# Kernel tuning notes

Measured on AMD Instinct MI355X. Metric: run time of the kernel, lower is better.

The kernel has to match this reference:

```python
import jax, jax.numpy as jnp
import numpy as np

B, S, D = 2, 4096, 1024
H, DK, DV = 4, 128, 256          # head_k_dim, head_v_dim
KD, VD = H * DK, H * DV          # key_dim=512, value_dim=1024
RANK = 16                        # gate_low_rank_dim
GLN = 16.0                       # gate_logit_normalizer
EPS = 1e-5
C = 64                           # chunk size
NC = S // C


def setup_inputs() -> dict:
    key = jax.random.key(0)
    ks = jax.random.split(key, 9)
    w = lambda k, shape: (jax.random.normal(k, shape, jnp.float32) * 0.02)
    return {
        "x": jax.random.normal(ks[0], (B, S, D), jnp.float32),
        "Wq": w(ks[1], (D, KD)),
        "Wk": w(ks[2], (D, KD)),
        "Wv": w(ks[3], (D, VD)),
        "Wgk1": w(ks[4], (D, RANK)),
        "Wgk2": w(ks[5], (RANK, KD)),
        "bgk": jnp.zeros((KD,), jnp.float32),
        "Wg": w(ks[6], (D, VD)),
        "Wo": w(ks[7], (VD, D)),
        "norm_w": jnp.ones((DV,), jnp.float32),
    }


def _gla_chunk(q, k, v, gk):
    """Chunkwise gated linear attention. q,k,gk: [B,S,H,DK]; v: [B,S,H,DV]."""
    qc = q.reshape(B, NC, C, H, DK)
    kc = k.reshape(B, NC, C, H, DK)
    vc = v.reshape(B, NC, C, H, DV)
    gc = gk.reshape(B, NC, C, H, DK)
    gcum = jnp.cumsum(gc, axis=2)                       # inclusive within-chunk cumsum (<= 0)
    g_last = gcum[:, :, -1]                             # [B,NC,H,DK]
    q_t = qc * jnp.exp(gcum)                            # q decayed forward
    k_inv = kc * jnp.exp(-gcum)                         # for intra-chunk scores
    k_dec = kc * jnp.exp(g_last[:, :, None] - gcum)     # for state update (bounded)
    # intra-chunk causal scores
    A = jnp.einsum('bnthk,bnshk->bnhts', q_t, k_inv)    # [B,NC,H,C,C]
    mask = jnp.tril(jnp.ones((C, C), bool))
    A = jnp.where(mask, A, 0.0)
    o_intra = jnp.einsum('bnhts,bnshv->bnthv', A, vc)   # [B,NC,C,H,DV]
    # per-chunk state contribution
    kv = jnp.einsum('bnthk,bnthv->bnhkv', k_dec, vc)    # [B,NC,H,DK,DV]

    def step(state, inp):
        q_tc, gl, kvc = inp                             # [B,C,H,DK], [B,H,DK], [B,H,DK,DV]
        o_inter = jnp.einsum('bthk,bhkv->bthv', q_tc, state)
        state = state * jnp.exp(gl)[..., None] + kvc
        return state, o_inter

    xs = (jnp.swapaxes(q_t, 0, 1), jnp.swapaxes(g_last, 0, 1), jnp.swapaxes(kv, 0, 1))
    init = jnp.zeros((B, H, DK, DV), q.dtype)
    _, o_inter = jax.lax.scan(step, init, xs)           # [NC,B,C,H,DV]
    o = o_intra + jnp.swapaxes(o_inter, 0, 1)
    return o.reshape(B, S, H, DV)


def reference(x, Wq, Wk, Wv, Wgk1, Wgk2, bgk, Wg, Wo, norm_w):
    scale = DK ** -0.5
    q = (x @ Wq).reshape(B, S, H, DK) * scale
    k = (x @ Wk).reshape(B, S, H, DK)
    v = (x @ Wv).reshape(B, S, H, DV)
    gk = (jax.nn.log_sigmoid((x @ Wgk1) @ Wgk2 + bgk) / GLN).reshape(B, S, H, DK)
    o = _gla_chunk(q, k, v, gk)                          # [B,S,H,DV]
    # fused RMSNorm + swish gate (per-head norm over DV)
    g = (x @ Wg).reshape(B, S, H, DV)
    o = o * jax.lax.rsqrt(jnp.mean(o * o, axis=-1, keepdims=True) + EPS) * norm_w
    o = o * (g * jax.nn.sigmoid(g))
    return o.reshape(B, S, VD) @ Wo
```

## Files before the change

kernel.cpp:

```cpp
#include <hip/hip_runtime.h>

typedef __bf16 bf16_t;
typedef __bf16 bf16x4 __attribute__((ext_vector_type(4)));
typedef __bf16 bf16x8 __attribute__((ext_vector_type(8)));
typedef float  f32x4  __attribute__((ext_vector_type(4)));

#define MFMA16(a,b,c) __builtin_amdgcn_mfma_f32_16x16x32_bf16((a),(b),(c),0,0,0)

#define SCALE_Q 0.08838834764831845f

#define GLOBAL_LOAD_LDS16(gptr, lptr)                                          \
  __builtin_amdgcn_global_load_lds(                                            \
      (const __attribute__((address_space(1))) void*)(gptr),                   \
      (__attribute__((address_space(3))) void*)(lptr), 16, 0, 0)

struct ConvSrcs {
  const void *wq, *wk, *wv, *wg, *wo, *gk1, *gk2, *bgk, *nw;
};
__device__ __forceinline__ void convT_tile(const void* src, bf16_t* dst,
                                           int Ccols, int bx, int by,
                                           bool isf32, bf16_t (*t)[33]) {
  int tx = threadIdx.x & 31, ty = threadIdx.x >> 5;
  int r0 = by * 32, c0 = bx * 32;
#pragma unroll
  for (int i = 0; i < 4; i++) {
    int r = r0 + ty + i * 8, cc = c0 + tx;
    float v = isf32 ? ((const float*)src)[(size_t)r * Ccols + cc]
                    : (float)((const bf16_t*)src)[(size_t)r * Ccols + cc];
    t[ty + i * 8][tx] = (bf16_t)v;
  }
  __syncthreads();
#pragma unroll
  for (int i = 0; i < 4; i++) {
    int cc = c0 + ty + i * 8;
    dst[(size_t)cc * 1024 + r0 + tx] = t[tx][ty + i * 8];
  }
}
__device__ __forceinline__ void conv_straight(const void* src, bf16_t* dst,
                                              int base_blk, int n, bool isf32) {
  int g = (blockIdx.x - base_blk) * 256 + threadIdx.x;
  int i = g * 8;
  if (i >= n) return;
  if (isf32) {
    const float4* s = (const float4*)src;
    float4 a = s[g * 2], b = s[g * 2 + 1];
    bf16x8 o;
    o[0] = (bf16_t)a.x; o[1] = (bf16_t)a.y; o[2] = (bf16_t)a.z; o[3] = (bf16_t)a.w;
    o[4] = (bf16_t)b.x; o[5] = (bf16_t)b.y; o[6] = (bf16_t)b.z; o[7] = (bf16_t)b.w;
    *(bf16x8*)(dst + i) = o;
  } else {
    *(bf16x8*)(dst + i) = ((const bf16x8*)src)[g];
  }
}
__global__ __launch_bounds__(256) void k_convW(ConvSrcs s,
                                               const unsigned int* __restrict__ nwp,
                                               bf16_t* __restrict__ tWcat,
                                               bf16_t* __restrict__ tWo,
                                               bf16_t* __restrict__ cWgk1,
                                               bf16_t* __restrict__ cWgk2,
                                               bf16_t* __restrict__ cbgk,
                                               bf16_t* __restrict__ cnw) {
  __shared__ bf16_t t[32][33];
  bool isf32 = (nwp[0] == 0x3F800000u);
  int blk = blockIdx.x;
  if (blk < 512) {
    convT_tile(s.wq, tWcat, 512, blk & 15, blk >> 4, isf32, t);
  } else if (blk < 1024) {
    int b2 = blk - 512;
    convT_tile(s.wk, tWcat + (size_t)512 * 1024, 512, b2 & 15, b2 >> 4, isf32, t);
  } else if (blk < 2048) {
    int b2 = blk - 1024;
    convT_tile(s.wv, tWcat + (size_t)1024 * 1024, 1024, b2 & 31, b2 >> 5, isf32, t);
  } else if (blk < 3072) {
    int b2 = blk - 2048;
    convT_tile(s.wg, tWcat + (size_t)2048 * 1024, 1024, b2 & 31, b2 >> 5, isf32, t);
  } else if (blk < 4096) {
    int b2 = blk - 3072;
    convT_tile(s.wo, tWo, 1024, b2 & 31, b2 >> 5, isf32, t);
  } else if (blk < 4104) {
    conv_straight(s.gk1, cWgk1, 4096, 16384, isf32);
  } else if (blk < 4108) {
    conv_straight(s.gk2, cWgk2, 4104, 8192, isf32);
  } else if (blk == 4108) {
    conv_straight(s.bgk, cbgk, 4108, 512, isf32);
  } else {
    conv_straight(s.nw, cnw, 4109, 256, isf32);
  }
}

__global__ __launch_bounds__(256) void k_gk1c(const void* __restrict__ src,
                                              const unsigned int* __restrict__ nwp,
                                              const bf16_t* __restrict__ W1,
                                              float* __restrict__ tmp,
                                              bf16_t* __restrict__ cx) {
  bool isf32 = (nwp[0] == 0x3F800000u);
  int wave = threadIdx.x >> 6, lane = threadIdx.x & 63;
  int m = blockIdx.x * 4 + wave;
  float p[16];
#pragma unroll
  for (int n = 0; n < 16; n++) p[n] = 0.f;
  for (int kk = 0; kk < 16; kk++) {
    int k = kk * 64 + lane;
    float raw = isf32 ? ((const float*)src)[(size_t)m * 1024 + k]
                      : (float)((const bf16_t*)src)[(size_t)m * 1024 + k];
    bf16_t bx = (bf16_t)raw;
    cx[(size_t)m * 1024 + k] = bx;
    float xv = (float)bx;
    bf16x8 w0 = *(const bf16x8*)(W1 + k * 16);
    bf16x8 w1 = *(const bf16x8*)(W1 + k * 16 + 8);
#pragma unroll
    for (int j = 0; j < 8; j++) {
      p[j]     += xv * (float)w0[j];
      p[8 + j] += xv * (float)w1[j];
    }
  }
#pragma unroll
  for (int off = 1; off < 64; off <<= 1) {
#pragma unroll
    for (int n = 0; n < 16; n++) p[n] += __shfl_xor(p[n], off, 64);
  }
#pragma unroll
  for (int n = 0; n < 16; n++)
    if (lane == n) tmp[(size_t)m * 16 + n] = p[n];
}

__global__ __launch_bounds__(128) void k_gkcum(const float* __restrict__ tmp,
                                               const bf16_t* __restrict__ W2,
                                               const bf16_t* __restrict__ bgk,
                                               float* __restrict__ gcum,
                                               float* __restrict__ glast,
                                               float* __restrict__ eglast) {
  __shared__ float lt[64][16];
  int blk = blockIdx.x;
  int bh = blk >> 6, n = blk & 63;
  int b = bh >> 2, h = bh & 3;
  int dk = threadIdx.x;
  int m0 = b * 4096 + n * 64;
  const float4* tsrc = (const float4*)(tmp + (size_t)m0 * 16);
  ((float4*)lt)[dk * 2]     = tsrc[dk * 2];
  ((float4*)lt)[dk * 2 + 1] = tsrc[dk * 2 + 1];
  int col = h * 128 + dk;
  float wv[16];
#pragma unroll
  for (int k = 0; k < 16; k++) wv[k] = (float)W2[k * 512 + col];
  float bv = (float)bgk[col];
  __syncthreads();
  float run = 0.f;
  float* dst = gcum + ((size_t)bh * 4096 + (size_t)n * 64) * 128 + dk;
  for (int t = 0; t < 64; t++) {
    float acc = 0.f;
#pragma unroll
    for (int k = 0; k < 16; k++) acc += lt[t][k] * wv[k];
    float z = acc + bv;
    float lg = -__logf(1.f + __expf(-z)) * (1.f / 16.f);
    run += fmaxf(lg, -4.0f);
    dst[t * 128] = run;
  }
  glast[(size_t)blk * 128 + dk] = run;
  eglast[(size_t)blk * 128 + dk] = __expf(run);
}

__global__ __launch_bounds__(512, 4) void k_gemm(const bf16_t* __restrict__ Ag,
                                              const bf16_t* __restrict__ Bt,
                                              int mode,
                                              const float* __restrict__ gcum,
                                              const float* __restrict__ glast,
                                              bf16_t* __restrict__ qt,
                                              bf16_t* __restrict__ kinv,
                                              bf16_t* __restrict__ kdecT,
                                              bf16_t* __restrict__ vrT,
                                              bf16_t* __restrict__ gmat,
                                              float* __restrict__ fout) {
  __shared__ __attribute__((aligned(16))) bf16_t As[2 * 256 * 32];
  __shared__ __attribute__((aligned(16))) bf16_t Bs[2 * 128 * 32];
  int tid = threadIdx.x;
  int w = tid >> 6, lane = tid & 63, quad = lane >> 4, c = lane & 15;
  int bid = blockIdx.x;
  int xcd = bid & 7, slot = bid >> 3;
  int bm, bn;
  if (mode == 0) { bm = xcd * 4 + slot / 24; bn = slot % 24; }
  else           { bm = xcd * 4 + (slot >> 3); bn = slot & 7; }
  int m0 = bm * 256, n0 = bn * 128;
  int WM = w >> 1, WN = w & 1;
  int r0s = w * 32 + (lane >> 2);
  int r1s = r0s + 16;
  int rbs = w * 16 + (lane >> 2);
  int s = lane & 3;
  int f0 = (s - (r0s >> 1)) & 3;
  int f1 = (s - (r1s >> 1)) & 3;
  int fb = (s - (rbs >> 1)) & 3;
  const bf16_t* a0 = Ag + (size_t)(m0 + r0s) * 1024 + f0 * 8;
  const bf16_t* a1 = Ag + (size_t)(m0 + r1s) * 1024 + f1 * 8;
  const bf16_t* b0 = Bt + (size_t)(n0 + rbs) * 1024 + fb * 8;
  bf16_t* lA = As + w * 1024;
  bf16_t* lB = Bs + w * 512;
  int raOff[4], rbOff[4];
#pragma unroll
  for (int t4 = 0; t4 < 4; t4++) {
    int ra = WM * 64 + t4 * 16 + c;
    raOff[t4] = ra * 32 + (((quad + (ra >> 1)) & 3) * 8);
    int rb = WN * 64 + t4 * 16 + c;
    rbOff[t4] = rb * 32 + (((quad + (rb >> 1)) & 3) * 8);
  }
  GLOBAL_LOAD_LDS16(a0, lA);
  GLOBAL_LOAD_LDS16(a1, lA + 512);
  GLOBAL_LOAD_LDS16(b0, lB);
  f32x4 acc[4][4] = {};
  for (int k0 = 0; k0 < 1024; k0 += 32) {
    __syncthreads();
    int cur = (k0 >> 5) & 1;
    int nxt = cur ^ 1;
    if (k0 + 32 < 1024) {
      GLOBAL_LOAD_LDS16(a0 + k0 + 32, lA + nxt * 8192);
      GLOBAL_LOAD_LDS16(a1 + k0 + 32, lA + nxt * 8192 + 512);
      GLOBAL_LOAD_LDS16(b0 + k0 + 32, lB + nxt * 4096);
    }
    bf16x8 af[4], bfr[4];
#pragma unroll
    for (int t4 = 0; t4 < 4; t4++) af[t4] = *(const bf16x8*)(As + cur * 8192 + raOff[t4]);
#pragma unroll
    for (int t4 = 0; t4 < 4; t4++) bfr[t4] = *(const bf16x8*)(Bs + cur * 4096 + rbOff[t4]);
#pragma unroll
    for (int mt = 0; mt < 4; mt++)
#pragma unroll
      for (int nt = 0; nt < 4; nt++)
        acc[mt][nt] = MFMA16(af[mt], bfr[nt], acc[mt][nt]);
  }
#pragma unroll
  for (int mt = 0; mt < 4; mt++)
#pragma unroll
    for (int nt = 0; nt < 4; nt++) {
      int mb = m0 + WM * 64 + mt * 16 + quad * 4;
      int n  = n0 + WN * 64 + nt * 16 + c;
      if (mode == 1) {
#pragma unroll
        for (int r = 0; r < 4; r++)
          fout[(size_t)(mb + r) * 1024 + n] = acc[mt][nt][r];
      } else if (n0 < 512) {
        int b = mb >> 12, ss0 = mb & 4095, h = n >> 7, dk = n & 127;
        size_t idx0 = ((size_t)(b * 4 + h) * 4096 + ss0) * 128 + dk;
#pragma unroll
        for (int r = 0; r < 4; r++)
          qt[idx0 + (size_t)r * 128] =
              (bf16_t)(acc[mt][nt][r] * SCALE_Q * __expf(gcum[idx0 + (size_t)r * 128]));
      } else if (n0 < 1024) {
        int nk = n - 512;
        int b = mb >> 12, ss0 = mb & 4095, h = nk >> 7, dk = nk & 127;
        int bh = b * 4 + h, chunk = ss0 >> 6, t0 = ss0 & 63;
        size_t idx0 = ((size_t)bh * 4096 + ss0) * 128 + dk;
        float gl = glast[((size_t)bh * 64 + chunk) * 128 + dk];
        bf16x4 kd;
#pragma unroll
        for (int r = 0; r < 4; r++) {
          float gc = gcum[idx0 + (size_t)r * 128];
          kinv[idx0 + (size_t)r * 128] =
              (bf16_t)(acc[mt][nt][r] * __expf(fminf(-gc, 30.f)));
          kd[r] = (bf16_t)(acc[mt][nt][r] * __expf(gl - gc));
        }
        *(bf16x4*)(kdecT + ((size_t)(bh * 64 + chunk) * 128 + dk) * 64 + t0) = kd;
      } else if (n0 < 2048) {
        int nv = n - 1024;
        int b = mb >> 12, ss0 = mb & 4095, h = nv >> 8, dv = nv & 255;
        int bh = b * 4 + h, chunk = ss0 >> 6, t0 = ss0 & 63;
        bf16x4 vv;
#pragma unroll
        for (int r = 0; r < 4; r++) vv[r] = (bf16_t)acc[mt][nt][r];
        *(bf16x4*)(vrT + ((size_t)(bh * 64 + chunk) * 256 + dv) * 64 + t0) = vv;
      } else {
#pragma unroll
        for (int r = 0; r < 4; r++)
          gmat[(size_t)(mb + r) * 1024 + (n - 2048)] = (bf16_t)acc[mt][nt][r];
      }
    }
}

__global__ __launch_bounds__(512, 4) void k_kv(const bf16_t* __restrict__ kdecT,
                                               const bf16_t* __restrict__ vrT,
                                               bf16_t* __restrict__ kv) {
  int blk = blockIdx.x;
  int tid = threadIdx.x, wave = tid >> 6, lane = tid & 63;
  int quad = lane >> 4, c = lane & 15;
  size_t cb = (size_t)blk * 8192;
  size_t cv = (size_t)blk * 16384;
  size_t sb = (size_t)blk * 32768;
  int dvbase = (wave >> 1) * 64;
  int kgbase = (wave & 1) * 64;
  f32x4 acc[4][4] = {};
  for (int kk = 0; kk < 64; kk += 32) {
    bf16x8 a[4], bb[4];
#pragma unroll
    for (int mt = 0; mt < 4; mt++)
      a[mt] = *(const bf16x8*)(vrT + cv + (size_t)(dvbase + mt * 16 + c) * 64 + kk + quad * 8);
#pragma unroll
    for (int nt = 0; nt < 4; nt++)
      bb[nt] = *(const bf16x8*)(kdecT + cb + (size_t)(kgbase + nt * 16 + c) * 64 + kk + quad * 8);
#pragma unroll
    for (int mt = 0; mt < 4; mt++)
#pragma unroll
      for (int nt = 0; nt < 4; nt++)
        acc[mt][nt] = MFMA16(a[mt], bb[nt], acc[mt][nt]);
  }
#pragma unroll
  for (int mt = 0; mt < 4; mt++)
#pragma unroll
    for (int nt = 0; nt < 4; nt++)
#pragma unroll
      for (int r = 0; r < 4; r++) {
        int dv = dvbase + mt * 16 + quad * 4 + r;
        int kg = kgbase + nt * 16 + c;
        kv[sb + (size_t)dv * 128 + kg] = (bf16_t)acc[mt][nt][r];
      }
}

__global__ __launch_bounds__(256) void k_scan2(bf16_t* __restrict__ states,
                                               const float* __restrict__ eglast) {
  int g = blockIdx.x * 256 + threadIdx.x;
  int bh = g >> 15;
  int idx = g & 32767;
  int kg = idx & 127;
  bf16_t* p = states + (size_t)bh * 64 * 32768 + idx;
  const float* egl = eglast + (size_t)bh * 64 * 128 + kg;
  float carry = 0.f;
#pragma unroll 4
  for (int n = 0; n < 64; n++) {
    float kvv = (float)p[(size_t)n * 32768];
    float e = egl[n * 128];
    p[(size_t)n * 32768] = (bf16_t)carry;
    carry = carry * e + kvv;
  }
}

__global__ __launch_bounds__(256, 4) void k_o2(const bf16_t* __restrict__ qt,
                                               const bf16_t* __restrict__ kinv,
                                               const bf16_t* __restrict__ vrT,
                                               const bf16_t* __restrict__ states,
                                               const bf16_t* __restrict__ gmat,
                                               const bf16_t* __restrict__ normw,
                                               bf16_t* __restrict__ ob) {
  int blk = blockIdx.x;
  int bh = blk >> 6, n = blk & 63, b = bh >> 2, h = bh & 3;
  __shared__ __attribute__((aligned(16))) bf16_t As[64 * 64];
  __shared__ __attribute__((aligned(16))) float lred[64][4];
  int tid = threadIdx.x, wave = tid >> 6, lane = tid & 63;
  int quad = lane >> 4, c = lane & 15;
  size_t cb = (size_t)blk * 8192;
  size_t cv = (size_t)blk * 16384;
  size_t sb = (size_t)blk * 32768;

  {
    f32x4 a4[4] = {};
    for (int kk = 0; kk < 128; kk += 32) {
      bf16x8 a = *(const bf16x8*)(qt + cb + (size_t)(wave * 16 + c) * 128 + kk + quad * 8);
#pragma unroll
      for (int nt = 0; nt < 4; nt++) {
        bf16x8 bb = *(const bf16x8*)(kinv + cb + (size_t)(nt * 16 + c) * 128 + kk + quad * 8);
        a4[nt] = MFMA16(a, bb, a4[nt]);
      }
    }
#pragma unroll
    for (int nt = 0; nt < 4; nt++)
#pragma unroll
      for (int r = 0; r < 4; r++) {
        int row = wave * 16 + quad * 4 + r, col = nt * 16 + c;
        As[row * 64 + (col ^ ((row & 7) * 8))] =
            (bf16_t)(col <= row ? a4[nt][r] : 0.f);
      }
  }
  __syncthreads();

  f32x4 acc[4][4] = {};
  for (int half = 0; half < 2; half++) {
    for (int kk2 = 0; kk2 < 2; kk2++) {
      int kg = half * 64 + kk2 * 32;
      bf16x8 a[4], bb[4];
#pragma unroll
      for (int mt = 0; mt < 4; mt++)
        a[mt] = *(const bf16x8*)(qt + cb + (size_t)(mt * 16 + c) * 128 + kg + quad * 8);
#pragma unroll
      for (int nt = 0; nt < 4; nt++)
        bb[nt] = *(const bf16x8*)(states + sb + (size_t)(wave * 64 + nt * 16 + c) * 128 + kg + quad * 8);
#pragma unroll
      for (int mt = 0; mt < 4; mt++)
#pragma unroll
        for (int nt = 0; nt < 4; nt++)
          acc[mt][nt] = MFMA16(a[mt], bb[nt], acc[mt][nt]);
    }
  }
  int akey = (c & 7) * 8;
  for (int kk = 0; kk < 64; kk += 32) {
    bf16x8 a[4], bb[4];
#pragma unroll
    for (int mt = 0; mt < 4; mt++)
      a[mt] = *(const bf16x8*)&As[(mt * 16 + c) * 64 + ((kk + quad * 8) ^ akey)];
#pragma unroll
    for (int nt = 0; nt < 4; nt++)
      bb[nt] = *(const bf16x8*)(vrT + cv + (size_t)(wave * 64 + nt * 16 + c) * 64 + kk + quad * 8);
#pragma unroll
    for (int mt = 0; mt < 4; mt++)
#pragma unroll
      for (int nt = 0; nt < 4; nt++)
        acc[mt][nt] = MFMA16(a[mt], bb[nt], acc[mt][nt]);
  }
  float p[4][4];
#pragma unroll
  for (int mt = 0; mt < 4; mt++)
#pragma unroll
    for (int r = 0; r < 4; r++) {
      float s = 0.f;
#pragma unroll
      for (int nt = 0; nt < 4; nt++) s += acc[mt][nt][r] * acc[mt][nt][r];
      p[mt][r] = s;
    }
#pragma unroll
  for (int off = 1; off < 16; off <<= 1) {
#pragma unroll
    for (int mt = 0; mt < 4; mt++)
#pragma unroll
      for (int r = 0; r < 4; r++) p[mt][r] += __shfl_xor(p[mt][r], off, 64);
  }
  if (c == 0) {
#pragma unroll
    for (int mt = 0; mt < 4; mt++)
#pragma unroll
      for (int r = 0; r < 4; r++) lred[mt * 16 + quad * 4 + r][wave] = p[mt][r];
  }
  __syncthreads();
#pragma unroll
  for (int mt = 0; mt < 4; mt++)
#pragma unroll
    for (int r = 0; r < 4; r++) {
      int row = mt * 16 + quad * 4 + r;
      float tot = lred[row][0] + lred[row][1] + lred[row][2] + lred[row][3];
      float rs = rsqrtf(tot * (1.f / 256.f) + 1e-5f);
      int sg = n * 64 + row;
      size_t gb = ((size_t)(b * 4096 + sg)) * 1024 + h * 256;
#pragma unroll
      for (int nt = 0; nt < 4; nt++) {
        int dv = wave * 64 + nt * 16 + c;
        float ov = acc[mt][nt][r] * rs * (float)normw[dv];
        float gv = (float)gmat[gb + dv];
        ov *= gv / (1.f + __expf(-gv));
        ob[gb + dv] = (bf16_t)ov;
      }
    }
}

extern "C" void kernel_launch(void* const* d_in, const int* in_sizes, int n_in,
                              void* d_out, int out_size, void* d_ws, size_t ws_size,
                              hipStream_t stream) {
  (void)in_sizes; (void)n_in; (void)out_size; (void)ws_size;
  const unsigned int* nw_oracle = (const unsigned int*)d_in[9];

  char* ws = (char*)d_ws;
  size_t off = 0;
  auto alloc = [&](size_t bytes) -> void* {
    void* p = ws + off;
    off += (bytes + 255) & ~(size_t)255;
    return p;
  };
  bf16_t* states = (bf16_t*)alloc((size_t)512 * 32768 * 2);
  bf16_t* cx     = states;
  float*  glast  = (float*) alloc((size_t)8 * 64 * 128 * 4);
  float*  eglast = (float*) alloc((size_t)8 * 64 * 128 * 4);
  float*  tmp    = (float*) alloc((size_t)8192 * 16 * 4);
  float*  gcum   = (float*) alloc((size_t)8 * 4096 * 128 * 4);
  bf16_t* ob     = (bf16_t*)gcum;
  bf16_t* qt     = (bf16_t*)alloc((size_t)8 * 4096 * 128 * 2);
  bf16_t* kinv   = (bf16_t*)alloc((size_t)8 * 4096 * 128 * 2);
  bf16_t* kdecT  = (bf16_t*)alloc((size_t)8 * 4096 * 128 * 2);
  bf16_t* vrT    = (bf16_t*)alloc((size_t)8 * 4096 * 256 * 2);
  bf16_t* gmat   = (bf16_t*)alloc((size_t)8192 * 1024 * 2);
  bf16_t* tWcat  = (bf16_t*)alloc((size_t)3072 * 1024 * 2);
  bf16_t* cWgk1  = (bf16_t*)alloc((size_t)1024 * 16 * 2);
  bf16_t* cWgk2  = (bf16_t*)alloc((size_t)16 * 512 * 2);
  bf16_t* cbgk   = (bf16_t*)alloc((size_t)512 * 2);
  bf16_t* tWo    = (bf16_t*)alloc((size_t)1024 * 1024 * 2);
  bf16_t* cnw    = (bf16_t*)alloc((size_t)256 * 2);

  ConvSrcs cs{d_in[1], d_in[2], d_in[3], d_in[7], d_in[8],
              d_in[4], d_in[5], d_in[6], d_in[9]};
  k_convW<<<4110, 256, 0, stream>>>(cs, nw_oracle, tWcat, tWo,
                                    cWgk1, cWgk2, cbgk, cnw);

  k_gk1c<<<2048, 256, 0, stream>>>(d_in[0], nw_oracle, cWgk1, tmp, cx);
  k_gkcum<<<512, 128, 0, stream>>>(tmp, cWgk2, cbgk, gcum, glast, eglast);
  k_gemm<<<768, 512, 0, stream>>>(cx, tWcat, 0, gcum, glast,
                                  qt, kinv, kdecT, vrT, gmat, nullptr);
  k_kv<<<512, 512, 0, stream>>>(kdecT, vrT, states);
  k_scan2<<<1024, 256, 0, stream>>>(states, eglast);
  k_o2<<<512, 256, 0, stream>>>(qt, kinv, vrT, states, gmat, cnw, ob);
  k_gemm<<<256, 512, 0, stream>>>(ob, tWo, 1, nullptr, nullptr,
                                  nullptr, nullptr, nullptr, nullptr, nullptr,
                                  (float*)d_out);
}
```

Measured before the change: 301.8 us.

## Fuse weight conversion with gate projection and add dedicated output GEMM kernel

Merges the weight-conversion kernel and the low-rank gate projection kernel into one launch. The gate projection now reads the original Wgk1 directly and converts it inline, which removes the dependency on the converted copy. It also replaces the mode-1 use of the large 256x128-tile GEMM for the output projection with a separate 128x128-tile kernel using 256 threads, giving 512 blocks instead of 256 for better CU occupancy. Dropping the mode branch also simplifies the main GEMM epilogue.

After: 307.0 us. About the same (+1.7%).

```diff
diff --git a/kernel.cpp b/kernel.cpp
--- a/kernel.cpp
+++ b/kernel.cpp
@@ -52,14 +52,17 @@
     *(bf16x8*)(dst + i) = ((const bf16x8*)src)[g];
   }
 }
-__global__ __launch_bounds__(256) void k_convW(ConvSrcs s,
+__global__ __launch_bounds__(256) void k_front(ConvSrcs s,
                                                const unsigned int* __restrict__ nwp,
                                                bf16_t* __restrict__ tWcat,
                                                bf16_t* __restrict__ tWo,
                                                bf16_t* __restrict__ cWgk1,
                                                bf16_t* __restrict__ cWgk2,
                                                bf16_t* __restrict__ cbgk,
-                                               bf16_t* __restrict__ cnw) {
+                                               bf16_t* __restrict__ cnw,
+                                               const void* __restrict__ xsrc,
+                                               float* __restrict__ tmp,
+                                               bf16_t* __restrict__ cx) {
   __shared__ bf16_t t[32][33];
   bool isf32 = (nwp[0] == 0x3F800000u);
   int blk = blockIdx.x;
@@ -83,45 +86,57 @@
     conv_straight(s.gk2, cWgk2, 4104, 8192, isf32);
   } else if (blk == 4108) {
     conv_straight(s.bgk, cbgk, 4108, 512, isf32);
+  } else if (blk == 4109) {
+    conv_straight(s.nw, cnw, 4109, 256, isf32);
   } else {
-    conv_straight(s.nw, cnw, 4109, 256, isf32);
-  }
-}
-
-__global__ __launch_bounds__(256) void k_gk1c(const void* __restrict__ src,
-                                              const unsigned int* __restrict__ nwp,
-                                              const bf16_t* __restrict__ W1,
-                                              float* __restrict__ tmp,
-                                              bf16_t* __restrict__ cx) {
-  bool isf32 = (nwp[0] == 0x3F800000u);
-  int wave = threadIdx.x >> 6, lane = threadIdx.x & 63;
-  int m = blockIdx.x * 4 + wave;
-  float p[16];
-#pragma unroll
-  for (int n = 0; n < 16; n++) p[n] = 0.f;
-  for (int kk = 0; kk < 16; kk++) {
-    int k = kk * 64 + lane;
-    float raw = isf32 ? ((const float*)src)[(size_t)m * 1024 + k]
-                      : (float)((const bf16_t*)src)[(size_t)m * 1024 + k];
-    bf16_t bx = (bf16_t)raw;
-    cx[(size_t)m * 1024 + k] = bx;
-    float xv = (float)bx;
-    bf16x8 w0 = *(const bf16x8*)(W1 + k * 16);
-    bf16x8 w1 = *(const bf16x8*)(W1 + k * 16 + 8);
-#pragma unroll
-    for (int j = 0; j < 8; j++) {
-      p[j]     += xv * (float)w0[j];
-      p[8 + j] += xv * (float)w1[j];
-    }
-  }
-#pragma unroll
-  for (int off = 1; off < 64; off <<= 1) {
-#pragma unroll
-    for (int n = 0; n < 16; n++) p[n] += __shfl_xor(p[n], off, 64);
-  }
-#pragma unroll
-  for (int n = 0; n < 16; n++)
-    if (lane == n) tmp[(size_t)m * 16 + n] = p[n];
+    int wave = threadIdx.x >> 6, lane = threadIdx.x & 63;
+    int m = (blk - 4110) * 4 + wave;
+    float p[16];
+#pragma unroll
+    for (int n = 0; n < 16; n++) p[n] = 0.f;
+    if (isf32) {
+      const float* xs = (const float*)xsrc;
+      const float* gw = (const float*)s.gk1;
+      for (int kk = 0; kk < 16; kk++) {
+        int k = kk * 64 + lane;
+        bf16_t bx = (bf16_t)xs[(size_t)m * 1024 + k];
+        cx[(size_t)m * 1024 + k] = bx;
+        float xv = (float)bx;
+        float4 wa = *(const float4*)(gw + k * 16);
+        float4 wb = *(const float4*)(gw + k * 16 + 4);
+        float4 wc = *(const float4*)(gw + k * 16 + 8);
+        float4 wd = *(const float4*)(gw + k * 16 + 12);
+        float wv[16] = {wa.x, wa.y, wa.z, wa.w, wb.x, wb.y, wb.z, wb.w,
+                        wc.x, wc.y, wc.z, wc.w, wd.x, wd.y, wd.z, wd.w};
+#pragma unroll
+        for (int j = 0; j < 16; j++) p[j] += xv * (float)(bf16_t)wv[j];
+      }
+    } else {
+      const bf16_t* xs = (const bf16_t*)xsrc;
+      const bf16_t* gw = (const bf16_t*)s.gk1;
+      for (int kk = 0; kk < 16; kk++) {
+        int k = kk * 64 + lane;
+        bf16_t bx = xs[(size_t)m * 1024 + k];
+        cx[(size_t)m * 1024 + k] = bx;
+        float xv = (float)bx;
+        bf16x8 w0 = *(const bf16x8*)(gw + k * 16);
+        bf16x8 w1 = *(const bf16x8*)(gw + k * 16 + 8);
+#pragma unroll
+        for (int j = 0; j < 8; j++) {
+          p[j]     += xv * (float)w0[j];
+          p[8 + j] += xv * (float)w1[j];
+        }
+      }
+    }
+#pragma unroll
+    for (int off = 1; off < 64; off <<= 1) {
+#pragma unroll
+      for (int n = 0; n < 16; n++) p[n] += __shfl_xor(p[n], off, 64);
+    }
+#pragma unroll
+    for (int n = 0; n < 16; n++)
+      if (lane == n) tmp[(size_t)m * 16 + n] = p[n];
+  }
 }
 
 __global__ __launch_bounds__(128) void k_gkcum(const float* __restrict__ tmp,
@@ -162,24 +177,20 @@
 
 __global__ __launch_bounds__(512, 4) void k_gemm(const bf16_t* __restrict__ Ag,
                                               const bf16_t* __restrict__ Bt,
-                                              int mode,
                                               const float* __restrict__ gcum,
                                               const float* __restrict__ glast,
                                               bf16_t* __restrict__ qt,
                                               bf16_t* __restrict__ kinv,
                                               bf16_t* __restrict__ kdecT,
                                               bf16_t* __restrict__ vrT,
-                                              bf16_t* __restrict__ gmat,
-                                              float* __restrict__ fout) {
+                                              bf16_t* __restrict__ gmat) {
   __shared__ __attribute__((aligned(16))) bf16_t As[2 * 256 * 32];
   __shared__ __attribute__((aligned(16))) bf16_t Bs[2 * 128 * 32];
   int tid = threadIdx.x;
   int w = tid >> 6, lane = tid & 63, quad = lane >> 4, c = lane & 15;
   int bid = blockIdx.x;
   int xcd = bid & 7, slot = bid >> 3;
-  int bm, bn;
-  if (mode == 0) { bm = xcd * 4 + slot / 24; bn = slot % 24; }
-  else           { bm = xcd * 4 + (slot >> 3); bn = slot & 7; }
+  int bm = xcd * 4 + slot / 24, bn = slot % 24;
   int m0 = bm * 256, n0 = bn * 128;
   int WM = w >> 1, WN = w & 1;
   int r0s = w * 32 + (lane >> 2);
@@ -232,11 +243,7 @@
     for (int nt = 0; nt < 4; nt++) {
       int mb = m0 + WM * 64 + mt * 16 + quad * 4;
       int n  = n0 + WN * 64 + nt * 16 + c;
-      if (mode == 1) {
-#pragma unroll
-        for (int r = 0; r < 4; r++)
-          fout[(size_t)(mb + r) * 1024 + n] = acc[mt][nt][r];
-      } else if (n0 < 512) {
+      if (n0 < 512) {
         int b = mb >> 12, ss0 = mb & 4095, h = n >> 7, dk = n & 127;
         size_t idx0 = ((size_t)(b * 4 + h) * 4096 + ss0) * 128 + dk;
 #pragma unroll
@@ -272,6 +279,73 @@
           gmat[(size_t)(mb + r) * 1024 + (n - 2048)] = (bf16_t)acc[mt][nt][r];
       }
     }
+}
+
+__global__ __launch_bounds__(256, 4) void k_gemm1(const bf16_t* __restrict__ Ag,
+                                                  const bf16_t* __restrict__ Bt,
+                                                  float* __restrict__ fout) {
+  __shared__ __attribute__((aligned(16))) bf16_t As[2 * 128 * 32];
+  __shared__ __attribute__((aligned(16))) bf16_t Bs[2 * 128 * 32];
+  int tid = threadIdx.x;
+  int wave = tid >> 6, lane = tid & 63, quad = lane >> 4, c = lane & 15;
+  int m0 = blockIdx.y * 128, n0 = blockIdx.x * 128;
+  int wm = (wave >> 1) * 64, wn = (wave & 1) * 64;
+  int r0s = wave * 32 + (lane >> 2);
+  int r1s = r0s + 16;
+  int s = lane & 3;
+  int f0 = (s - (r0s >> 1)) & 3;
+  int f1 = (s - (r1s >> 1)) & 3;
+  const bf16_t* a0 = Ag + (size_t)(m0 + r0s) * 1024 + f0 * 8;
+  const bf16_t* a1 = Ag + (size_t)(m0 + r1s) * 1024 + f1 * 8;
+  const bf16_t* b0 = Bt + (size_t)(n0 + r0s) * 1024 + f0 * 8;
+  const bf16_t* b1 = Bt + (size_t)(n0 + r1s) * 1024 + f1 * 8;
+  bf16_t* lA = As + wave * 1024;
+  bf16_t* lB = Bs + wave * 1024;
+  int raOff[4], rbOff[4];
+#pragma unroll
+  for (int t4 = 0; t4 < 4; t4++) {
+    int ra = wm + t4 * 16 + c;
+    raOff[t4] = ra * 32 + (((quad + (ra >> 1)) & 3) * 8);
+    int rb = wn + t4 * 16 + c;
+    rbOff[t4] = rb * 32 + (((quad + (rb >> 1)) & 3) * 8);
+  }
+  GLOBAL_LOAD_LDS16(a0, lA);
+  GLOBAL_LOAD_LDS16(a1, lA + 512);
+  GLOBAL_LOAD_LDS16(b0, lB);
+  GLOBAL_LOAD_LDS16(b1, lB + 512);
+  f32x4 acc[4][4] = {};
+  for (int k0 = 0; k0 < 1024; k0 += 32) {
+    __syncthreads();
+    int cur = (k0 >> 5) & 1;
+    int nxtoff = (cur ^ 1) * 4096;
+    if (k0 + 32 < 1024) {
+      GLOBAL_LOAD_LDS16(a0 + k0 + 32, lA + nxtoff);
+      GLOBAL_LOAD_LDS16(a1 + k0 + 32, lA + nxtoff + 512);
+      GLOBAL_LOAD_LDS16(b0 + k0 + 32, lB + nxtoff);
+      GLOBAL_LOAD_LDS16(b1 + k0 + 32, lB + nxtoff + 512);
+    }
+    int curoff = cur * 4096;
+    bf16x8 af[4], bfr[4];
+#pragma unroll
+    for (int t4 = 0; t4 < 4; t4++) af[t4] = *(const bf16x8*)(As + curoff + raOff[t4]);
+#pragma unroll
+    for (int t4 = 0; t4 < 4; t4++) bfr[t4] = *(const bf16x8*)(Bs + curoff + rbOff[t4]);
+#pragma unroll
+    for (int mt = 0; mt < 4; mt++)
+#pragma unroll
+      for (int nt = 0; nt < 4; nt++)
+        acc[mt][nt] = MFMA16(af[mt], bfr[nt], acc[mt][nt]);
+  }
+#pragma unroll
+  for (int mt = 0; mt < 4; mt++)
+#pragma unroll
+    for (int nt = 0; nt < 4; nt++)
+#pragma unroll
+      for (int r = 0; r < 4; r++) {
+        int m = m0 + wm + mt * 16 + quad * 4 + r;
+        int n = n0 + wn + nt * 16 + c;
+        fout[(size_t)m * 1024 + n] = acc[mt][nt][r];
+      }
 }
 
 __global__ __launch_bounds__(512, 4) void k_kv(const bf16_t* __restrict__ kdecT,
@@ -479,17 +553,14 @@
 
   ConvSrcs cs{d_in[1], d_in[2], d_in[3], d_in[7], d_in[8],
               d_in[4], d_in[5], d_in[6], d_in[9]};
-  k_convW<<<4110, 256, 0, stream>>>(cs, nw_oracle, tWcat, tWo,
-                                    cWgk1, cWgk2, cbgk, cnw);
-
-  k_gk1c<<<2048, 256, 0, stream>>>(d_in[0], nw_oracle, cWgk1, tmp, cx);
+  k_front<<<6158, 256, 0, stream>>>(cs, nw_oracle, tWcat, tWo,
+                                    cWgk1, cWgk2, cbgk, cnw,
+                                    d_in[0], tmp, cx);
   k_gkcum<<<512, 128, 0, stream>>>(tmp, cWgk2, cbgk, gcum, glast, eglast);
-  k_gemm<<<768, 512, 0, stream>>>(cx, tWcat, 0, gcum, glast,
-                                  qt, kinv, kdecT, vrT, gmat, nullptr);
+  k_gemm<<<768, 512, 0, stream>>>(cx, tWcat, gcum, glast,
+                                  qt, kinv, kdecT, vrT, gmat);
   k_kv<<<512, 512, 0, stream>>>(kdecT, vrT, states);
   k_scan2<<<1024, 256, 0, stream>>>(states, eglast);
   k_o2<<<512, 256, 0, stream>>>(qt, kinv, vrT, states, gmat, cnw, ob);
-  k_gemm<<<256, 512, 0, stream>>>(ob, tWo, 1, nullptr, nullptr,
-                                  nullptr, nullptr, nullptr, nullptr, nullptr,
-                                  (float*)d_out);
-}
+  k_gemm1<<<dim3(8, 64), 256, 0, stream>>>(ob, tWo, (float*)d_out);
+}
```
